# Kernel optimization log

Hardware: AMD Instinct MI355X
Metric: run time of the kernel (lower is better)

The kernel has to match this reference:

```python
import jax, jax.numpy as jnp
import numpy as np
from jax import lax

B, T, D = 2, 1024, 2048
HK, HV = 8, 16          # num key heads / num value heads
DK, DV = 128, 128       # head dims
KW = 4                  # conv kernel size
EPS = 1e-6
KEY_DIM = HK * DK
VALUE_DIM = HV * DV
CONV_DIM = 2 * KEY_DIM + VALUE_DIM


def setup_inputs() -> dict:
    key = jax.random.key(0)
    ks = jax.random.split(key, 9)
    w = lambda k, shape, s=0.02: jax.random.normal(k, shape, jnp.float32) * s
    return {
        'hidden_states': jax.random.normal(ks[0], (B, T, D), jnp.float32),
        'W_qkv': w(ks[1], (D, CONV_DIM)),
        'W_z': w(ks[2], (D, VALUE_DIM)),
        'W_b': w(ks[3], (D, HV)),
        'W_a': w(ks[4], (D, HV)),
        'conv_w': w(ks[5], (CONV_DIM, KW), 0.5),
        'dt_bias': jnp.ones((HV,), jnp.float32),
        'A_log': jnp.log(jax.random.uniform(ks[6], (HV,), jnp.float32, 1e-3, 16.0)),
        'norm_weight': jnp.ones((DV,), jnp.float32),
        'W_out': w(ks[7], (VALUE_DIM, D)),
    }


def _causal_conv_silu(x, w):
    # x: [B, C, T], w: [C, K] depthwise causal conv + SiLU (causal_conv1d_fn)
    k = w.shape[1]
    xp = jnp.pad(x, ((0, 0), (0, 0), (k - 1, 0)))
    y = sum(w[:, j][None, :, None] * xp[:, :, j:j + x.shape[2]] for j in range(k))
    return jax.nn.silu(y)


def _l2norm(x):
    return x * lax.rsqrt(jnp.sum(x * x, -1, keepdims=True) + 1e-6)


def reference(hidden_states, W_qkv, W_z, W_b, W_a, conv_w, dt_bias, A_log,
              norm_weight, W_out):
    Bb, Tt, _ = hidden_states.shape
    mixed = hidden_states @ W_qkv                       # [B,T,conv_dim]
    mixed = _causal_conv_silu(mixed.transpose(0, 2, 1), conv_w).transpose(0, 2, 1)
    q, k, v = jnp.split(mixed, [KEY_DIM, 2 * KEY_DIM], axis=-1)
    q = q.reshape(Bb, Tt, HK, DK)
    k = k.reshape(Bb, Tt, HK, DK)
    v = v.reshape(Bb, Tt, HV, DV)
    z = (hidden_states @ W_z).reshape(Bb, Tt, HV, DV)
    beta = jax.nn.sigmoid(hidden_states @ W_b)          # [B,T,HV]
    g = -jnp.exp(A_log) * jax.nn.softplus(hidden_states @ W_a + dt_bias)  # [B,T,HV]

    rep = HV // HK  # GQA: repeat_interleave q,k heads
    q = jnp.repeat(q, rep, axis=2)
    k = jnp.repeat(k, rep, axis=2)
    q = _l2norm(q) * (DK ** -0.5)                       # use_qk_l2norm + scale
    k = _l2norm(k)

    # gated delta-rule recurrence (fp32 state), scanned over time
    qs = q.transpose(1, 0, 2, 3)   # [T,B,HV,DK]
    ks = k.transpose(1, 0, 2, 3)
    vs = v.transpose(1, 0, 2, 3)   # [T,B,HV,DV]
    gs = g.transpose(1, 0, 2)      # [T,B,HV]
    bs = beta.transpose(1, 0, 2)

    def step(S, inp):
        qt, kt, vt, gt, bt = inp
        S = S * jnp.exp(gt)[..., None, None]                          # decay
        v_adj = (vt - jnp.einsum('bhk,bhkv->bhv', kt, S)) * bt[..., None]
        S = S + kt[..., None] * v_adj[..., None, :]                   # rank-1 delta update
        o = jnp.einsum('bhk,bhkv->bhv', qt, S)
        return S, o

    S0 = jnp.zeros((Bb, HV, DK, DV), jnp.float32)
    _, o = lax.scan(step, S0, (qs, ks, vs, gs, bs))
    o = o.transpose(1, 0, 2, 3)                         # [B,T,HV,DV]

    # gated RMSNorm over head_v_dim
    var = jnp.mean(o * o, -1, keepdims=True)
    o = o * lax.rsqrt(var + EPS) * norm_weight
    o = o * jax.nn.silu(z)

    return o.reshape(Bb, Tt, VALUE_DIM) @ W_out         # [B,T,D]
```

## Files before the change

kernel.cpp:

```cpp
#include <hip/hip_runtime.h>
#include <hip/hip_bf16.h>

#define B_ 2
#define T_ 1024
#define D_ 2048
#define HK_ 8
#define HV_ 16
#define DK_ 128
#define DV_ 128
#define KEY_DIM_ 1024
#define VALUE_DIM_ 2048
#define CONV_DIM_ 4096
#define BT_ 2048
#define NCH_ 16
#define CL_ 64

typedef __attribute__((ext_vector_type(8))) short short8;
typedef __attribute__((ext_vector_type(4))) float f32x4;

__device__ __forceinline__ short f2bf(float x) {
  __hip_bfloat16 h = __float2bfloat16(x);
  return *reinterpret_cast<short*>(&h);
}
__device__ __forceinline__ float bf2f(short u) {
  unsigned int x = ((unsigned int)(unsigned short)u) << 16;
  return __int_as_float(x);
}

#define GLOAD_LDS16(g, l)                                             \
  __builtin_amdgcn_global_load_lds(                                   \
      (const __attribute__((address_space(1))) void*)(g),             \
      (__attribute__((address_space(3))) void*)(l), 16, 0, 0)

__global__ void transpose_cast(const float* __restrict__ W, short* __restrict__ WT, int R, int C) {
  __shared__ float tile[32][33];
  int tx = threadIdx.x, ty = threadIdx.y;
  int x = blockIdx.x * 32 + tx;
#pragma unroll
  for (int j = 0; j < 4; ++j) {
    int r = blockIdx.y * 32 + ty + j * 8;
    tile[ty + j * 8][tx] = W[(long)r * C + x];
  }
  __syncthreads();
  int ro = blockIdx.y * 32 + tx;
#pragma unroll
  for (int j = 0; j < 4; ++j) {
    int co = blockIdx.x * 32 + ty + j * 8;
    WT[(long)co * R + ro] = f2bf(tile[tx][ty + j * 8]);
  }
}

__global__ void interleave_ba(const float* __restrict__ Wb, const float* __restrict__ Wa,
                              float* __restrict__ Wba32) {
  int i = blockIdx.x * 256 + threadIdx.x;
  int c = i & 31, k = i >> 5;
  Wba32[i] = (c < 16) ? Wb[k * 16 + c] : Wa[k * 16 + (c - 16)];
}

__global__ __launch_bounds__(512) void gemm256_split(const short* __restrict__ A,
                                                     const short* __restrict__ Bt,
                                                     float* __restrict__ C0,
                                                     float* __restrict__ C1,
                                                     int N0, int N1, int K) {
  __shared__ short lds[65536];
  const int tid = threadIdx.x;
  const int lane = tid & 63, wid = tid >> 6;
  const int quad = lane >> 4, l16 = lane & 15;
  const int wm = (wid >> 2) * 128, wn = (wid & 3) * 64;
  const int m0 = blockIdx.y * 256, n0 = blockIdx.x * 256;

  const int r8 = tid >> 3, t8 = (tid & 7) * 8;
  const int csw = t8 ^ ((r8 & 7) << 3);
  const int rB = (r8 & 31) + ((r8 >> 5) << 6);
  const int cswr = (quad ^ (l16 & 7)) << 3;
  const int NT = K >> 6, NIT = NT >> 1;

  f32x4 acc[8][4] = {};
  short8 a[4][2], bl[2][2], bh[2][2];

#define SGA(p, kt, rb)                                                        \
  GLOAD_LDS16(A + (long)(m0 + (rb) + r8) * K + (kt) * 64 + csw,               \
              lds + (p) * 32768 + ((rb) + r8) * 64 + t8)
#define SGB(p, kt, rb)                                                        \
  GLOAD_LDS16(Bt + (long)(n0 + (rb) + rB) * K + (kt) * 64 + csw,              \
              lds + (p) * 32768 + 16384 + ((rb) + rB) * 64 + t8)
#define UA0(p, kt) do { SGA(p, kt, 0);  SGA(p, kt, 128); } while (0)
#define UA2(p, kt) do { SGA(p, kt, 64); SGA(p, kt, 192); } while (0)
#define UB1(p, kt) do { SGB(p, kt, 0);  SGB(p, kt, 128); } while (0)
#define UB3(p, kt) do { SGB(p, kt, 32); SGB(p, kt, 160); } while (0)
#define RDA(p, r, kk) (*(const short8*)(lds + (p) * 32768 + (r) * 64 + (cswr ^ ((kk) << 5))))
#define RDB(p, r, kk) (*(const short8*)(lds + (p) * 32768 + 16384 + (r) * 64 + (cswr ^ ((kk) << 5))))
#define MFMA_(d, x, y) d = __builtin_amdgcn_mfma_f32_16x16x32_bf16(x, y, d, 0, 0, 0)
#define BAR_() do { __builtin_amdgcn_s_barrier(); __builtin_amdgcn_sched_barrier(0); } while (0)
#define PRIO_ON_() __builtin_amdgcn_s_setprio(1)
#define PRIO_OFF_() do { __builtin_amdgcn_s_setprio(0); __builtin_amdgcn_sched_barrier(0); } while (0)

  UA0(0, 0); UB1(0, 0); UA2(0, 0); UB3(0, 0);
  UA0(1, 1); UB1(1, 1); UA2(1, 1);
  asm volatile("s_waitcnt vmcnt(6)" ::: "memory");
  BAR_();

#pragma unroll 1
  for (int i = 0; i < NIT; ++i) {
    const int tb = 2 * i + 1, tc = 2 * i + 2, td = 2 * i + 3;
    const bool more = (i + 1 < NIT);

#pragma unroll
    for (int mi = 0; mi < 4; ++mi) {
      a[mi][0] = RDA(0, wm + mi * 16 + l16, 0);
      a[mi][1] = RDA(0, wm + mi * 16 + l16, 1);
    }
#pragma unroll
    for (int ni = 0; ni < 2; ++ni) {
      bl[ni][0] = RDB(0, wn + ni * 16 + l16, 0);
      bl[ni][1] = RDB(0, wn + ni * 16 + l16, 1);
    }
    UB3(1, tb);
    BAR_();
    PRIO_ON_();
#pragma unroll
    for (int mi = 0; mi < 4; ++mi)
#pragma unroll
      for (int ni = 0; ni < 2; ++ni) {
        MFMA_(acc[mi][ni], a[mi][0], bl[ni][0]);
        MFMA_(acc[mi][ni], a[mi][1], bl[ni][1]);
      }
    PRIO_OFF_();
    __builtin_amdgcn_s_barrier();

    __builtin_amdgcn_sched_barrier(0);
#pragma unroll
    for (int ni = 0; ni < 2; ++ni) {
      bh[ni][0] = RDB(0, wn + 32 + ni * 16 + l16, 0);
      bh[ni][1] = RDB(0, wn + 32 + ni * 16 + l16, 1);
    }
    if (more) UA0(0, tc);
    BAR_();
    PRIO_ON_();
#pragma unroll
    for (int mi = 0; mi < 4; ++mi)
#pragma unroll
      for (int ni = 0; ni < 2; ++ni) {
        MFMA_(acc[mi][2 + ni], a[mi][0], bh[ni][0]);
        MFMA_(acc[mi][2 + ni], a[mi][1], bh[ni][1]);
      }
    PRIO_OFF_();
    __builtin_amdgcn_s_barrier();

    __builtin_amdgcn_sched_barrier(0);
#pragma unroll
    for (int mi = 0; mi < 4; ++mi) {
      a[mi][0] = RDA(0, wm + 64 + mi * 16 + l16, 0);
      a[mi][1] = RDA(0, wm + 64 + mi * 16 + l16, 1);
    }
    if (more) UB1(0, tc);
    BAR_();
    PRIO_ON_();
#pragma unroll
    for (int mi = 0; mi < 4; ++mi)
#pragma unroll
      for (int ni = 0; ni < 2; ++ni) {
        MFMA_(acc[4 + mi][2 + ni], a[mi][0], bh[ni][0]);
        MFMA_(acc[4 + mi][2 + ni], a[mi][1], bh[ni][1]);
      }
    PRIO_OFF_();
    __builtin_amdgcn_s_barrier();

    __builtin_amdgcn_sched_barrier(0);
    if (more) UA2(0, tc);
    BAR_();
    PRIO_ON_();
#pragma unroll
    for (int mi = 0; mi < 4; ++mi)
#pragma unroll
      for (int ni = 0; ni < 2; ++ni) {
        MFMA_(acc[4 + mi][ni], a[mi][0], bl[ni][0]);
        MFMA_(acc[4 + mi][ni], a[mi][1], bl[ni][1]);
      }
    PRIO_OFF_();
    if (more) { asm volatile("s_waitcnt vmcnt(6)" ::: "memory"); }
    else      { asm volatile("s_waitcnt vmcnt(0)" ::: "memory"); }
    __builtin_amdgcn_s_barrier();

    __builtin_amdgcn_sched_barrier(0);
#pragma unroll
    for (int mi = 0; mi < 4; ++mi) {
      a[mi][0] = RDA(1, wm + mi * 16 + l16, 0);
      a[mi][1] = RDA(1, wm + mi * 16 + l16, 1);
    }
#pragma unroll
    for (int ni = 0; ni < 2; ++ni) {
      bl[ni][0] = RDB(1, wn + ni * 16 + l16, 0);
      bl[ni][1] = RDB(1, wn + ni * 16 + l16, 1);
    }
    if (more) UB3(0, tc);
    BAR_();
    PRIO_ON_();
#pragma unroll
    for (int mi = 0; mi < 4; ++mi)
#pragma unroll
      for (int ni = 0; ni < 2; ++ni) {
        MFMA_(acc[mi][ni], a[mi][0], bl[ni][0]);
        MFMA_(acc[mi][ni], a[mi][1], bl[ni][1]);
      }
    PRIO_OFF_();
    __builtin_amdgcn_s_barrier();

    __builtin_amdgcn_sched_barrier(0);
#pragma unroll
    for (int ni = 0; ni < 2; ++ni) {
      bh[ni][0] = RDB(1, wn + 32 + ni * 16 + l16, 0);
      bh[ni][1] = RDB(1, wn + 32 + ni * 16 + l16, 1);
    }
    if (more) UA0(1, td);
    BAR_();
    PRIO_ON_();
#pragma unroll
    for (int mi = 0; mi < 4; ++mi)
#pragma unroll
      for (int ni = 0; ni < 2; ++ni) {
        MFMA_(acc[mi][2 + ni], a[mi][0], bh[ni][0]);
        MFMA_(acc[mi][2 + ni], a[mi][1], bh[ni][1]);
      }
    PRIO_OFF_();
    __builtin_amdgcn_s_barrier();

    __builtin_amdgcn_sched_barrier(0);
#pragma unroll
    for (int mi = 0; mi < 4; ++mi) {
      a[mi][0] = RDA(1, wm + 64 + mi * 16 + l16, 0);
      a[mi][1] = RDA(1, wm + 64 + mi * 16 + l16, 1);
    }
    if (more) UB1(1, td);
    BAR_();
    PRIO_ON_();
#pragma unroll
    for (int mi = 0; mi < 4; ++mi)
#pragma unroll
      for (int ni = 0; ni < 2; ++ni) {
        MFMA_(acc[4 + mi][2 + ni], a[mi][0], bh[ni][0]);
        MFMA_(acc[4 + mi][2 + ni], a[mi][1], bh[ni][1]);
      }
    PRIO_OFF_();
    __builtin_amdgcn_s_barrier();

    __builtin_amdgcn_sched_barrier(0);
    if (more) UA2(1, td);
    BAR_();
    PRIO_ON_();
#pragma unroll
    for (int mi = 0; mi < 4; ++mi)
#pragma unroll
      for (int ni = 0; ni < 2; ++ni) {
        MFMA_(acc[4 + mi][ni], a[mi][0], bl[ni][0]);
        MFMA_(acc[4 + mi][ni], a[mi][1], bl[ni][1]);
      }
    PRIO_OFF_();
    if (more) { asm volatile("s_waitcnt vmcnt(6)" ::: "memory"); }
    else      { asm volatile("s_waitcnt vmcnt(0)" ::: "memory"); }
    __builtin_amdgcn_s_barrier();
    __builtin_amdgcn_sched_barrier(0);
  }

  float* Cw; int ldc, cb;
  if (n0 < N0) { Cw = C0; ldc = N0; cb = n0; }
  else         { Cw = C1; ldc = N1; cb = n0 - N0; }
#pragma unroll
  for (int mi = 0; mi < 8; ++mi)
#pragma unroll
    for (int ni = 0; ni < 4; ++ni)
#pragma unroll
      for (int r = 0; r < 4; ++r) {
        int row = m0 + wm + mi * 16 + quad * 4 + r;
        int col = cb + wn + ni * 16 + l16;
        Cw[(long)row * ldc + col] = acc[mi][ni][r];
      }
#undef SGA
#undef SGB
#undef UA0
#undef UA2
#undef UB1
#undef UB3
#undef RDA
#undef RDB
#undef MFMA_
#undef BAR_
#undef PRIO_ON_
#undef PRIO_OFF_
}

__global__ __launch_bounds__(256) void gemm128_ks(const short* __restrict__ A,
                                                  const short* __restrict__ Bt,
                                                  float* __restrict__ Cp,
                                                  int M, int N, int K) {
  __shared__ short As[2][128 * 32];
  __shared__ short Bs[2][128 * 32];
  int m0 = blockIdx.y * 128, n0 = blockIdx.x * 128;
  int kh = K >> 1;
  int kbeg = blockIdx.z * kh;
  int tid = threadIdx.x;
  int wave = tid >> 6, lane = tid & 63;
  int wm = (wave >> 1) * 64, wn = (wave & 1) * 64;
  int quad = lane >> 4, l16 = lane & 15;
  f32x4 acc[4][4] = {};

  int ar = tid >> 2;
  int ac = (tid & 3) * 8;
  const short* Ag0 = A + (long)(m0 + ar) * K + ac + kbeg;
  const short* Ag1 = A + (long)(m0 + 64 + ar) * K + ac + kbeg;
  const short* Bg0 = Bt + (long)(n0 + ar) * K + ac + kbeg;
  const short* Bg1 = Bt + (long)(n0 + 64 + ar) * K + ac + kbeg;
  int NT = kh >> 5;

#define STAGE_(t, c)                                  \
  do {                                                \
    GLOAD_LDS16(Ag0 + (t) * 32, As[c] + tid * 8);     \
    GLOAD_LDS16(Ag1 + (t) * 32, As[c] + 64 * 32 + tid * 8); \
    GLOAD_LDS16(Bg0 + (t) * 32, Bs[c] + tid * 8);     \
    GLOAD_LDS16(Bg1 + (t) * 32, Bs[c] + 64 * 32 + tid * 8); \
  } while (0)

  STAGE_(0, 0);
  STAGE_(1, 1);

  for (int t = 0; t < NT; ++t) {
    int c = t & 1;
    if (t + 1 < NT) {
      asm volatile("s_waitcnt vmcnt(4)" ::: "memory");
    } else {
      asm volatile("s_waitcnt vmcnt(0)" ::: "memory");
    }
    __builtin_amdgcn_s_barrier();
    __builtin_amdgcn_sched_barrier(0);

    short8 af[4], bf_[4];
#pragma unroll
    for (int i = 0; i < 4; ++i) af[i] = *(const short8*)(As[c] + (wm + i * 16 + l16) * 32 + quad * 8);
#pragma unroll
    for (int j = 0; j < 4; ++j) bf_[j] = *(const short8*)(Bs[c] + (wn + j * 16 + l16) * 32 + quad * 8);
#pragma unroll
    for (int i = 0; i < 4; ++i)
#pragma unroll
      for (int j = 0; j < 4; ++j)
        acc[i][j] = __builtin_amdgcn_mfma_f32_16x16x32_bf16(af[i], bf_[j], acc[i][j], 0, 0, 0);

    __builtin_amdgcn_sched_barrier(0);
    __builtin_amdgcn_s_barrier();
    if (t + 2 < NT) STAGE_(t + 2, c);
  }

  float* Cz = Cp + (long)blockIdx.z * M * N;
#pragma unroll
  for (int i = 0; i < 4; ++i)
#pragma unroll
    for (int j = 0; j < 4; ++j)
#pragma unroll
      for (int r = 0; r < 4; ++r) {
        int row = m0 + wm + i * 16 + quad * 4 + r;
        int colx = n0 + wn + j * 16 + l16;
        Cz[(long)row * N + colx] = acc[i][j][r];
      }
#undef STAGE_
}

__global__ void add2(const float* __restrict__ p0, const float* __restrict__ p1,
                     float* __restrict__ out, int n4) {
  int i = blockIdx.x * 256 + threadIdx.x;
  if (i < n4) {
    float4 a = ((const float4*)p0)[i];
    float4 b = ((const float4*)p1)[i];
    float4 o;
    o.x = a.x + b.x; o.y = a.y + b.y; o.z = a.z + b.z; o.w = a.w + b.w;
    ((float4*)out)[i] = o;
  }
}

__global__ __launch_bounds__(256) void small_proj(const float* __restrict__ hidden,
                                                  const float* __restrict__ Wba32,
                                                  const float* __restrict__ dt_bias,
                                                  const float* __restrict__ A_log,
                                                  float* __restrict__ betaT,
                                                  float* __restrict__ gT,
                                                  short* __restrict__ hbf) {
  __shared__ float red[2][32][33];
  int r0 = blockIdx.x * 2;
  int tid = threadIdx.x;
  int cg = tid & 7, s = tid >> 3;
  const f32x4* wp = (const f32x4*)Wba32 + (long)s * 64 * 8 + cg;
  const f32x4* h0 = (const f32x4*)(hidden + (long)r0 * D_ + s * 64);
  const f32x4* h1 = (const f32x4*)(hidden + (long)(r0 + 1) * D_ + s * 64);
  f32x4 a0 = {0.f, 0.f, 0.f, 0.f}, a1 = {0.f, 0.f, 0.f, 0.f};
#pragma unroll
  for (int ii = 0; ii < 16; ++ii) {
    f32x4 ha = h0[ii], hb = h1[ii];
    f32x4 w0 = wp[(ii * 4 + 0) * 8];
    f32x4 w1 = wp[(ii * 4 + 1) * 8];
    f32x4 w2 = wp[(ii * 4 + 2) * 8];
    f32x4 w3 = wp[(ii * 4 + 3) * 8];
    a0 += ha[0] * w0; a1 += hb[0] * w0;
    a0 += ha[1] * w1; a1 += hb[1] * w1;
    a0 += ha[2] * w2; a1 += hb[2] * w2;
    a0 += ha[3] * w3; a1 += hb[3] * w3;
  }
#pragma unroll
  for (int j = 0; j < 4; ++j) {
    red[0][s][cg * 4 + j] = a0[j];
    red[1][s][cg * 4 + j] = a1[j];
  }
  {
    int colb = s * 64 + cg * 8;
    const float* p0 = hidden + (long)r0 * D_ + colb;
    const float* p1 = p0 + D_;
    float4 x0 = *(const float4*)(p0);
    float4 x1 = *(const float4*)(p0 + 4);
    float4 y0 = *(const float4*)(p1);
    float4 y1 = *(const float4*)(p1 + 4);
    short8 o0, o1;
    o0[0] = f2bf(x0.x); o0[1] = f2bf(x0.y); o0[2] = f2bf(x0.z); o0[3] = f2bf(x0.w);
    o0[4] = f2bf(x1.x); o0[5] = f2bf(x1.y); o0[6] = f2bf(x1.z); o0[7] = f2bf(x1.w);
    o1[0] = f2bf(y0.x); o1[1] = f2bf(y0.y); o1[2] = f2bf(y0.z); o1[3] = f2bf(y0.w);
    o1[4] = f2bf(y1.x); o1[5] = f2bf(y1.y); o1[6] = f2bf(y1.z); o1[7] = f2bf(y1.w);
    *(short8*)(hbf + (long)r0 * D_ + colb) = o0;
    *(short8*)(hbf + (long)(r0 + 1) * D_ + colb) = o1;
  }
  __syncthreads();
  if (tid < 64) {
    int row = tid >> 5, c = tid & 31;
    float t0 = 0.f, t1 = 0.f, t2 = 0.f, t3 = 0.f;
#pragma unroll
    for (int ss = 0; ss < 32; ss += 4) {
      t0 += red[row][ss][c];
      t1 += red[row][ss + 1][c];
      t2 += red[row][ss + 2][c];
      t3 += red[row][ss + 3][c];
    }
    float t = (t0 + t1) + (t2 + t3);
    int r = r0 + row;
    if (c < 16) {
      betaT[c * BT_ + r] = 1.f / (1.f + __expf(-t));
    } else {
      int hh = c - 16;
      float y = t + dt_bias[hh];
      float sp = fmaxf(y, 0.f) + log1pf(__expf(-fabsf(y)));
      gT[hh * BT_ + r] = -__expf(A_log[hh]) * sp;
    }
  }
}

__global__ void conv_silu(const float* __restrict__ x, const float* __restrict__ w,
                          float* __restrict__ y) {
  int idx = blockIdx.x * 256 + threadIdx.x;
  int c = idx & (CONV_DIM_ - 1);
  int bt = idx >> 12;
  int t = bt & (T_ - 1);
  float4 wc = *(const float4*)(w + c * 4);
  const float* xp = x + (long)idx;
  float acc = wc.w * xp[0];
  if (t >= 1) acc += wc.z * xp[-CONV_DIM_];
  if (t >= 2) acc += wc.y * xp[-2 * CONV_DIM_];
  if (t >= 3) acc += wc.x * xp[-3 * CONV_DIM_];
  y[idx] = acc * (1.f / (1.f + __expf(-acc)));
}

__global__ __launch_bounds__(64) void qknorm(const float* __restrict__ qkv,
                                             short* __restrict__ qb, short* __restrict__ kb) {
  int bi = blockIdx.x;
  int which = bi & 1;
  int h = (bi >> 1) & 7;
  int bt = bi >> 4;
  int lane = threadIdx.x;
  const float* src = qkv + (long)bt * CONV_DIM_ + which * KEY_DIM_ + h * DK_;
  float2 v = *(const float2*)(src + lane * 2);
  float ss = v.x * v.x + v.y * v.y;
#pragma unroll
  for (int m = 32; m; m >>= 1) ss += __shfl_xor(ss, m, 64);
  float scale = rsqrtf(ss + 1e-6f);
  if (which == 0) scale *= 0.08838834764831845f;
  short* dst = (which ? kb : qb) + ((long)bt * HK_ + h) * DK_;
  short2 o; o.x = f2bf(v.x * scale); o.y = f2bf(v.y * scale);
  ((short2*)dst)[lane] = o;
}

__global__ __launch_bounds__(256, 2) void chunk_phase1(
    const short* __restrict__ qbf, const short* __restrict__ kbf,
    const float* __restrict__ qkv, const float* __restrict__ gT,
    const float* __restrict__ bT,
    short* __restrict__ Pm, short* __restrict__ GQ, short* __restrict__ KtT,
    short* __restrict__ Wneg, float* __restrict__ Ut, float* __restrict__ Gammac) {
  __shared__ float Al[64 * 64];
  __shared__ float Gs[64], Gam[64], Dd[64], Bet[64], BG[64];

  int ci = blockIdx.x;
  int c = ci & 15, hv = (ci >> 4) & 15, b = ci >> 8;
  int hk = hv >> 1;
  int t0 = c * CL_;
  int tid = threadIdx.x;
  int wave = tid >> 6, lane = tid & 63, quad = lane >> 4, l16 = lane & 15;

  if (tid < 64) {
    float g = gT[(hv * B_ + b) * T_ + t0 + tid];
    float x = g;
#pragma unroll
    for (int off = 1; off < 64; off <<= 1) {
      float y = __shfl_up(x, off, 64);
      if (tid >= off) x += y;
    }
    Gs[tid] = x;
    float gm = __expf(x);
    Gam[tid] = gm;
    float Gtot = __shfl(x, 63, 64);
    Dd[tid] = __expf(Gtot - x);
    float bb = bT[(hv * B_ + b) * T_ + t0 + tid];
    Bet[tid] = bb;
    BG[tid] = bb * gm;
    if (tid == 63) Gammac[ci] = __expf(x);
// ... 151 lines not shown
      for (int kk = 0; kk < 4; ++kk)
        Wn[kk] = *(const short8*)(Wneg + cj * 8192 + (16 * wave + l16) * 128 + kk * 32 + quad * 8);
      const float* up = Ut + cj * 8192 + (16 * wave + quad * 4) * 128 + n0 + l16;
#pragma unroll
      for (int r = 0; r < 4; ++r) Un[r] = up[r * 128];
#pragma unroll
      for (int kk = 0; kk < 2; ++kk)
#pragma unroll
        for (int i = 0; i < 2; ++i)
          Kn[kk][i] = *(const short8*)(KtT + cj * 8192 + (32 * wave + 16 * i + l16) * 64 + kk * 32 + quad * 8);
    }
    __syncthreads();
    f32x4 Ua = Ur;
#pragma unroll
    for (int kk = 0; kk < 4; ++kk) {
      short8 bfv = *(const short8*)(SLT + l16 * 136 + kk * 32 + quad * 8);
      Ua = __builtin_amdgcn_mfma_f32_16x16x32_bf16(Wr[kk], bfv, Ua, 0, 0, 0);
    }
    {
      int s0 = 16 * wave + quad * 4;
      short4 p;
      p.x = f2bf(Ua[0]); p.y = f2bf(Ua[1]); p.z = f2bf(Ua[2]); p.w = f2bf(Ua[3]);
      *(short4*)(ULT + l16 * 72 + s0) = p;
      *(short4*)(UTg + ci * 8192 + (n0 + l16) * 64 + s0) = p;
    }
    __syncthreads();
    float gc = Gammac[ci];
#pragma unroll
    for (int i = 0; i < 2; ++i)
#pragma unroll
      for (int r = 0; r < 4; ++r) S2[i][r] *= gc;
#pragma unroll
    for (int kk = 0; kk < 2; ++kk) {
      short8 bfv = *(const short8*)(ULT + l16 * 72 + kk * 32 + quad * 8);
#pragma unroll
      for (int i = 0; i < 2; ++i)
        S2[i] = __builtin_amdgcn_mfma_f32_16x16x32_bf16(Kr[kk][i], bfv, S2[i], 0, 0, 0);
    }
    __syncthreads();
    if (ch + 1 < NCH_) {
#pragma unroll
      for (int kk = 0; kk < 4; ++kk) Wr[kk] = Wn[kk];
      Ur = Un;
#pragma unroll
      for (int kk = 0; kk < 2; ++kk)
#pragma unroll
        for (int i = 0; i < 2; ++i) Kr[kk][i] = Kn[kk][i];
    }
  }
}

__global__ __launch_bounds__(256) void chunk_phase3(
    const short* __restrict__ GQ, const short* __restrict__ ScTg,
    const short* __restrict__ Pm, const short* __restrict__ UTg,
    const float* __restrict__ zbuf, const float* __restrict__ nw,
    short* __restrict__ obf) {
  int ci = blockIdx.x;
  int c = ci & 15, hv = (ci >> 4) & 15, b = ci >> 8;
  int t0 = c * CL_;
  int tid = threadIdx.x, wave = tid >> 6, lane = tid & 63, quad = lane >> 4, l16 = lane & 15;
  f32x4 acc[8] = {};
#pragma unroll
  for (int kk = 0; kk < 4; ++kk) {
    short8 af = *(const short8*)(GQ + (long)ci * 8192 + (16 * wave + l16) * 128 + kk * 32 + quad * 8);
#pragma unroll
    for (int j = 0; j < 8; ++j) {
      short8 bfv = *(const short8*)(ScTg + (long)ci * 16384 + (16 * j + l16) * 128 + kk * 32 + quad * 8);
      acc[j] = __builtin_amdgcn_mfma_f32_16x16x32_bf16(af, bfv, acc[j], 0, 0, 0);
    }
  }
#pragma unroll
  for (int kk = 0; kk < 2; ++kk) {
    short8 af = *(const short8*)(Pm + (long)ci * 4096 + (16 * wave + l16) * 64 + kk * 32 + quad * 8);
#pragma unroll
    for (int j = 0; j < 8; ++j) {
      short8 bfv = *(const short8*)(UTg + (long)ci * 8192 + (16 * j + l16) * 64 + kk * 32 + quad * 8);
      acc[j] = __builtin_amdgcn_mfma_f32_16x16x32_bf16(af, bfv, acc[j], 0, 0, 0);
    }
  }
#pragma unroll
  for (int r = 0; r < 4; ++r) {
    float ss = 0.f;
#pragma unroll
    for (int j = 0; j < 8; ++j) ss += acc[j][r] * acc[j][r];
    ss += __shfl_xor(ss, 1, 64);
    ss += __shfl_xor(ss, 2, 64);
    ss += __shfl_xor(ss, 4, 64);
    ss += __shfl_xor(ss, 8, 64);
    float scale = rsqrtf(ss * (1.f / 128.f) + 1e-6f);
    int t = t0 + 16 * wave + quad * 4 + r;
    long base = (long)(b * T_ + t) * VALUE_DIM_ + hv * DV_;
#pragma unroll
    for (int j = 0; j < 8; ++j) {
      int n = 16 * j + l16;
      float zv = zbuf[base + n];
      float sz = zv * (1.f / (1.f + __expf(-zv)));
      obf[base + n] = f2bf(acc[j][r] * scale * nw[n] * sz);
    }
  }
}

extern "C" void kernel_launch(void* const* d_in, const int* in_sizes, int n_in,
                              void* d_out, int out_size, void* d_ws, size_t ws_size,
                              hipStream_t stream) {
  const float* hidden  = (const float*)d_in[0];
  const float* W_qkv   = (const float*)d_in[1];
  const float* W_z     = (const float*)d_in[2];
  const float* W_b     = (const float*)d_in[3];
  const float* W_a     = (const float*)d_in[4];
  const float* conv_w  = (const float*)d_in[5];
  const float* dt_bias = (const float*)d_in[6];
  const float* A_log   = (const float*)d_in[7];
  const float* norm_w  = (const float*)d_in[8];
  const float* W_out   = (const float*)d_in[9];
  float* out = (float*)d_out;

  char* ws = (char*)d_ws;
  size_t off = 0;
  auto alloc = [&](size_t bytes) {
    void* p = ws + off;
    off += (bytes + 255) & ~(size_t)255;
    return p;
  };
  short* hidden_bf = (short*)alloc((size_t)BT_ * D_ * 2);
  short* WcatT     = (short*)alloc((size_t)(CONV_DIM_ + VALUE_DIM_) * D_ * 2);
  short* WoutT     = (short*)alloc((size_t)D_ * VALUE_DIM_ * 2);
  float* mixed     = (float*)alloc((size_t)BT_ * CONV_DIM_ * 4);
  float* qkv       = (float*)alloc((size_t)BT_ * CONV_DIM_ * 4);
  float* zbuf      = (float*)alloc((size_t)BT_ * VALUE_DIM_ * 4);
  short* qbf       = (short*)alloc((size_t)BT_ * KEY_DIM_ * 2);
  short* kbf       = (short*)alloc((size_t)BT_ * KEY_DIM_ * 2);
  float* betab     = (float*)alloc((size_t)BT_ * HV_ * 4);
  float* gb        = (float*)alloc((size_t)BT_ * HV_ * 4);
  float* Wba32     = (float*)alloc((size_t)D_ * 32 * 4);
  short* Wneg      = (short*)alloc((size_t)512 * 8192 * 2);
  float* Ut32      = (float*)alloc((size_t)512 * 8192 * 4);
  short* KtT       = (short*)alloc((size_t)512 * 8192 * 2);
  short* UTg       = (short*)alloc((size_t)512 * 8192 * 2);
  short* ScTg      = (short*)alloc((size_t)512 * 16384 * 2);
  float* Gammac    = (float*)alloc((size_t)512 * 4);
  short* Pm   = (short*)(mixed + (size_t)BT_ * VALUE_DIM_);
  short* GQ   = Pm + (size_t)512 * 4096;
  short* obf  = hidden_bf;
  float* Cpart = qkv;

  dim3 tb32(32, 8);
  transpose_cast<<<dim3(CONV_DIM_ / 32, D_ / 32), tb32, 0, stream>>>(W_qkv, WcatT, D_, CONV_DIM_);
  transpose_cast<<<dim3(VALUE_DIM_ / 32, D_ / 32), tb32, 0, stream>>>(W_z, WcatT + (size_t)CONV_DIM_ * D_, D_, VALUE_DIM_);
  transpose_cast<<<dim3(D_ / 32, VALUE_DIM_ / 32), tb32, 0, stream>>>(W_out, WoutT, VALUE_DIM_, D_);
  interleave_ba<<<32 * D_ / 256, 256, 0, stream>>>(W_b, W_a, Wba32);

  small_proj<<<BT_ / 2, 256, 0, stream>>>(hidden, Wba32, dt_bias, A_log, betab, gb, hidden_bf);

  gemm256_split<<<dim3((CONV_DIM_ + VALUE_DIM_) / 256, BT_ / 256), 512, 0, stream>>>(
      hidden_bf, WcatT, mixed, zbuf, CONV_DIM_, VALUE_DIM_, D_);
  conv_silu<<<BT_ * CONV_DIM_ / 256, 256, 0, stream>>>(mixed, conv_w, qkv);
  qknorm<<<BT_ * HK_ * 2, 64, 0, stream>>>(qkv, qbf, kbf);

  chunk_phase1<<<512, 256, 0, stream>>>(qbf, kbf, qkv, gb, betab, Pm, GQ, KtT, Wneg, Ut32, Gammac);
  chunk_phase2<<<256, 256, 0, stream>>>(Wneg, Ut32, KtT, Gammac, UTg, ScTg);
  chunk_phase3<<<512, 256, 0, stream>>>(GQ, ScTg, Pm, UTg, zbuf, norm_w, obf);

  gemm128_ks<<<dim3(D_ / 128, BT_ / 128, 2), 256, 0, stream>>>(obf, WoutT, Cpart, BT_, D_, VALUE_DIM_);
  add2<<<(BT_ * D_ / 4 + 255) / 256, 256, 0, stream>>>(Cpart, Cpart + (size_t)BT_ * D_, out, BT_ * D_ / 4);
}
```

Baseline: 379.2 us.

## Retile input GEMM to 256x192 and port output GEMM to pipelined 256x128 kernel

The fused QKV/Z projection GEMM now uses 256x192 tiles instead of 256x256. That gives 32x8=256 blocks rather than 24x8=192, for better CU coverage on the device, with a per-column split when writing to the two outputs. The output projection replaces the simple 128x128 double-buffered split-K kernel with a 512-thread 256x128 version of the swizzled, barrier-phased pipeline. The cost is a smaller per-block reuse ratio, a more complex staging schedule, and tuned vmcnt counts that must match the number of loads in flight.

```diff
diff --git a/kernel.cpp b/kernel.cpp
--- a/kernel.cpp
+++ b/kernel.cpp
@@ -57,46 +57,42 @@
   Wba32[i] = (c < 16) ? Wb[k * 16 + c] : Wa[k * 16 + (c - 16)];
 }
 
-__global__ __launch_bounds__(512) void gemm256_split(const short* __restrict__ A,
-                                                     const short* __restrict__ Bt,
-                                                     float* __restrict__ C0,
-                                                     float* __restrict__ C1,
-                                                     int N0, int N1, int K) {
-  __shared__ short lds[65536];
-  const int tid = threadIdx.x;
-  const int lane = tid & 63, wid = tid >> 6;
-  const int quad = lane >> 4, l16 = lane & 15;
-  const int wm = (wid >> 2) * 128, wn = (wid & 3) * 64;
-  const int m0 = blockIdx.y * 256, n0 = blockIdx.x * 256;
-
-  const int r8 = tid >> 3, t8 = (tid & 7) * 8;
-  const int csw = t8 ^ ((r8 & 7) << 3);
-  const int rB = (r8 & 31) + ((r8 >> 5) << 6);
-  const int cswr = (quad ^ (l16 & 7)) << 3;
-  const int NT = K >> 6, NIT = NT >> 1;
-
-  f32x4 acc[8][4] = {};
-  short8 a[4][2], bl[2][2], bh[2][2];
-
-#define SGA(p, kt, rb)                                                        \
-  GLOAD_LDS16(A + (long)(m0 + (rb) + r8) * K + (kt) * 64 + csw,               \
-              lds + (p) * 32768 + ((rb) + r8) * 64 + t8)
-#define SGB(p, kt, rb)                                                        \
-  GLOAD_LDS16(Bt + (long)(n0 + (rb) + rB) * K + (kt) * 64 + csw,              \
-              lds + (p) * 32768 + 16384 + ((rb) + rB) * 64 + t8)
-#define UA0(p, kt) do { SGA(p, kt, 0);  SGA(p, kt, 128); } while (0)
-#define UA2(p, kt) do { SGA(p, kt, 64); SGA(p, kt, 192); } while (0)
-#define UB1(p, kt) do { SGB(p, kt, 0);  SGB(p, kt, 128); } while (0)
-#define UB3(p, kt) do { SGB(p, kt, 32); SGB(p, kt, 160); } while (0)
-#define RDA(p, r, kk) (*(const short8*)(lds + (p) * 32768 + (r) * 64 + (cswr ^ ((kk) << 5))))
-#define RDB(p, r, kk) (*(const short8*)(lds + (p) * 32768 + 16384 + (r) * 64 + (cswr ^ ((kk) << 5))))
 #define MFMA_(d, x, y) d = __builtin_amdgcn_mfma_f32_16x16x32_bf16(x, y, d, 0, 0, 0)
 #define BAR_() do { __builtin_amdgcn_s_barrier(); __builtin_amdgcn_sched_barrier(0); } while (0)
 #define PRIO_ON_() __builtin_amdgcn_s_setprio(1)
 #define PRIO_OFF_() do { __builtin_amdgcn_s_setprio(0); __builtin_amdgcn_sched_barrier(0); } while (0)
 
-  UA0(0, 0); UB1(0, 0); UA2(0, 0); UB3(0, 0);
-  UA0(1, 1); UB1(1, 1); UA2(1, 1);
+__global__ __launch_bounds__(512) void gemm256n192(const short* __restrict__ A,
+                                                   const short* __restrict__ Bt,
+                                                   float* __restrict__ C0,
+                                                   float* __restrict__ C1,
+                                                   int N0, int N1, int K) {
+  __shared__ short lds[57344];
+  const int tid = threadIdx.x;
+  const int lane = tid & 63, wid = tid >> 6;
+  const int quad = lane >> 4, l16 = lane & 15;
+  const int wm = (wid >> 1) * 64, wn = (wid & 1) * 96;
+  const int m0 = blockIdx.y * 256, n0 = blockIdx.x * 192;
+
+  const int r8 = tid >> 3, t8 = (tid & 7) * 8;
+  const int csw = t8 ^ ((r8 & 7) << 3);
+  const int cswr = (quad ^ (l16 & 7)) << 3;
+  const int NIT = K >> 7;
+
+  f32x4 acc[4][6] = {};
+  short8 a[4][2], bl[3][2], bh[3][2];
+
+#define SGA(p, kt, rb) GLOAD_LDS16(A + (long)(m0 + (rb) + r8) * K + (kt) * 64 + csw, \
+                                   lds + (p) * 28672 + ((rb) + r8) * 64 + t8)
+#define SGB(p, kt, rb) GLOAD_LDS16(Bt + (long)(n0 + (rb) + r8) * K + (kt) * 64 + csw, \
+                                   lds + (p) * 28672 + 16384 + ((rb) + r8) * 64 + t8)
+#define RDA(p, r, kk) (*(const short8*)(lds + (p) * 28672 + (r) * 64 + (cswr ^ ((kk) << 5))))
+#define RDB(p, r, kk) (*(const short8*)(lds + (p) * 28672 + 16384 + (r) * 64 + (cswr ^ ((kk) << 5))))
+
+  SGA(0, 0, 0); SGA(0, 0, 64); SGA(0, 0, 128); SGA(0, 0, 192);
+  SGB(0, 0, 0); SGB(0, 0, 64); SGB(0, 0, 128);
+  SGA(1, 1, 0); SGA(1, 1, 64); SGA(1, 1, 128); SGA(1, 1, 192);
+  SGB(1, 1, 0); SGB(1, 1, 64);
   asm volatile("s_waitcnt vmcnt(6)" ::: "memory");
   BAR_();
 
@@ -106,7 +102,220 @@
     const bool more = (i + 1 < NIT);
 
 #pragma unroll
-    for (int mi = 0; mi < 4; ++mi) {
+    for (int mi = 0; mi < 2; ++mi) {
+      a[mi][0] = RDA(0, wm + mi * 16 + l16, 0);
+      a[mi][1] = RDA(0, wm + mi * 16 + l16, 1);
+    }
+#pragma unroll
+    for (int ni = 0; ni < 3; ++ni) {
+      bl[ni][0] = RDB(0, wn + ni * 16 + l16, 0);
+      bl[ni][1] = RDB(0, wn + ni * 16 + l16, 1);
+    }
+    SGB(1, tb, 128);
+    BAR_();
+    PRIO_ON_();
+#pragma unroll
+    for (int mi = 0; mi < 2; ++mi)
+#pragma unroll
+      for (int ni = 0; ni < 3; ++ni) {
+        MFMA_(acc[mi][ni], a[mi][0], bl[ni][0]);
+        MFMA_(acc[mi][ni], a[mi][1], bl[ni][1]);
+      }
+    PRIO_OFF_();
+    __builtin_amdgcn_s_barrier();
+
+    __builtin_amdgcn_sched_barrier(0);
+#pragma unroll
+    for (int mi = 2; mi < 4; ++mi) {
+      a[mi][0] = RDA(0, wm + mi * 16 + l16, 0);
+      a[mi][1] = RDA(0, wm + mi * 16 + l16, 1);
+    }
+    BAR_();
+    PRIO_ON_();
+#pragma unroll
+    for (int mi = 2; mi < 4; ++mi)
+#pragma unroll
+      for (int ni = 0; ni < 3; ++ni) {
+        MFMA_(acc[mi][ni], a[mi][0], bl[ni][0]);
+        MFMA_(acc[mi][ni], a[mi][1], bl[ni][1]);
+      }
+    PRIO_OFF_();
+    __builtin_amdgcn_s_barrier();
+
+    __builtin_amdgcn_sched_barrier(0);
+#pragma unroll
+    for (int ni = 0; ni < 3; ++ni) {
+      bh[ni][0] = RDB(0, wn + 48 + ni * 16 + l16, 0);
+      bh[ni][1] = RDB(0, wn + 48 + ni * 16 + l16, 1);
+    }
+    if (more) { SGA(0, tc, 0); SGA(0, tc, 64); }
+    BAR_();
+    PRIO_ON_();
+#pragma unroll
+    for (int mi = 0; mi < 2; ++mi)
+#pragma unroll
+      for (int ni = 0; ni < 3; ++ni) {
+        MFMA_(acc[mi][3 + ni], a[mi][0], bh[ni][0]);
+        MFMA_(acc[mi][3 + ni], a[mi][1], bh[ni][1]);
+      }
+    PRIO_OFF_();
+    __builtin_amdgcn_s_barrier();
+
+    __builtin_amdgcn_sched_barrier(0);
+    if (more) { SGA(0, tc, 128); SGA(0, tc, 192); SGB(0, tc, 0); SGB(0, tc, 64); }
+    BAR_();
+    PRIO_ON_();
+#pragma unroll
+    for (int mi = 2; mi < 4; ++mi)
+#pragma unroll
+      for (int ni = 0; ni < 3; ++ni) {
+        MFMA_(acc[mi][3 + ni], a[mi][0], bh[ni][0]);
+        MFMA_(acc[mi][3 + ni], a[mi][1], bh[ni][1]);
+      }
+    PRIO_OFF_();
+    if (more) { asm volatile("s_waitcnt vmcnt(6)" ::: "memory"); }
+    else      { asm volatile("s_waitcnt vmcnt(0)" ::: "memory"); }
+    __builtin_amdgcn_s_barrier();
+
+    __builtin_amdgcn_sched_barrier(0);
+#pragma unroll
+    for (int mi = 0; mi < 2; ++mi) {
+      a[mi][0] = RDA(1, wm + mi * 16 + l16, 0);
+      a[mi][1] = RDA(1, wm + mi * 16 + l16, 1);
+    }
+#pragma unroll
+    for (int ni = 0; ni < 3; ++ni) {
+      bl[ni][0] = RDB(1, wn + ni * 16 + l16, 0);
+      bl[ni][1] = RDB(1, wn + ni * 16 + l16, 1);
+    }
+    if (more) SGB(0, tc, 128);
+    BAR_();
+    PRIO_ON_();
+#pragma unroll
+    for (int mi = 0; mi < 2; ++mi)
+#pragma unroll
+      for (int ni = 0; ni < 3; ++ni) {
+        MFMA_(acc[mi][ni], a[mi][0], bl[ni][0]);
+        MFMA_(acc[mi][ni], a[mi][1], bl[ni][1]);
+      }
+    PRIO_OFF_();
+    __builtin_amdgcn_s_barrier();
+
+    __builtin_amdgcn_sched_barrier(0);
+#pragma unroll
+    for (int mi = 2; mi < 4; ++mi) {
+      a[mi][0] = RDA(1, wm + mi * 16 + l16, 0);
+      a[mi][1] = RDA(1, wm + mi * 16 + l16, 1);
+    }
+    BAR_();
+    PRIO_ON_();
+#pragma unroll
+    for (int mi = 2; mi < 4; ++mi)
+#pragma unroll
+      for (int ni = 0; ni < 3; ++ni) {
+        MFMA_(acc[mi][ni], a[mi][0], bl[ni][0]);
+        MFMA_(acc[mi][ni], a[mi][1], bl[ni][1]);
+      }
+    PRIO_OFF_();
+    __builtin_amdgcn_s_barrier();
+
+    __builtin_amdgcn_sched_barrier(0);
+#pragma unroll
+    for (int ni = 0; ni < 3; ++ni) {
+      bh[ni][0] = RDB(1, wn + 48 + ni * 16 + l16, 0);
+      bh[ni][1] = RDB(1, wn + 48 + ni * 16 + l16, 1);
+    }
+    if (more) { SGA(1, td, 0); SGA(1, td, 64); }
+    BAR_();
+    PRIO_ON_();
+#pragma unroll
+    for (int mi = 0; mi < 2; ++mi)
+#pragma unroll
+      for (int ni = 0; ni < 3; ++ni) {
+        MFMA_(acc[mi][3 + ni], a[mi][0], bh[ni][0]);
+        MFMA_(acc[mi][3 + ni], a[mi][1], bh[ni][1]);
+      }
+    PRIO_OFF_();
+    __builtin_amdgcn_s_barrier();
+
+    __builtin_amdgcn_sched_barrier(0);
+    if (more) { SGA(1, td, 128); SGA(1, td, 192); SGB(1, td, 0); SGB(1, td, 64); }
+    BAR_();
+    PRIO_ON_();
+#pragma unroll
+    for (int mi = 2; mi < 4; ++mi)
+#pragma unroll
+      for (int ni = 0; ni < 3; ++ni) {
+        MFMA_(acc[mi][3 + ni], a[mi][0], bh[ni][0]);
+        MFMA_(acc[mi][3 + ni], a[mi][1], bh[ni][1]);
+      }
+    PRIO_OFF_();
+    if (more) { asm volatile("s_waitcnt vmcnt(6)" ::: "memory"); }
+    else      { asm volatile("s_waitcnt vmcnt(0)" ::: "memory"); }
+    __builtin_amdgcn_s_barrier();
+    __builtin_amdgcn_sched_barrier(0);
+  }
+
+#pragma unroll
+  for (int mi = 0; mi < 4; ++mi)
+#pragma unroll
+    for (int ni = 0; ni < 6; ++ni)
+#pragma unroll
+      for (int r = 0; r < 4; ++r) {
+        int row = m0 + wm + mi * 16 + quad * 4 + r;
+        int col = n0 + wn + ni * 16 + l16;
+        if (col < N0) C0[(long)row * N0 + col] = acc[mi][ni][r];
+        else          C1[(long)row * N1 + (col - N0)] = acc[mi][ni][r];
+      }
+#undef SGA
+#undef SGB
+#undef RDA
+#undef RDB
+}
+
+__global__ __launch_bounds__(512) void gemm256ks(const short* __restrict__ Ag,
+                                                 const short* __restrict__ Btg,
+                                                 float* __restrict__ Cp,
+                                                 int M, int N, int K) {
+  __shared__ short lds[49152];
+  const int tid = threadIdx.x;
+  const int lane = tid & 63, wid = tid >> 6;
+  const int quad = lane >> 4, l16 = lane & 15;
+  const int wm = (wid >> 1) * 64, wn = (wid & 1) * 64;
+  const int m0 = blockIdx.y * 256, n0 = blockIdx.x * 128;
+  const int kh = K >> 1;
+  const short* A = Ag + blockIdx.z * kh;
+  const short* Bt = Btg + blockIdx.z * kh;
+
+  const int r8 = tid >> 3, t8 = (tid & 7) * 8;
+  const int csw = t8 ^ ((r8 & 7) << 3);
+  const int cswr = (quad ^ (l16 & 7)) << 3;
+  const int NIT = kh >> 7;
+
+  f32x4 acc[4][4] = {};
+  short8 a[4][2], bl[2][2], bh[2][2];
+
+#define SGA(p, kt, rb) GLOAD_LDS16(A + (long)(m0 + (rb) + r8) * K + (kt) * 64 + csw, \
+                                   lds + (p) * 24576 + ((rb) + r8) * 64 + t8)
+#define SGB(p, kt, rb) GLOAD_LDS16(Bt + (long)(n0 + (rb) + r8) * K + (kt) * 64 + csw, \
+                                   lds + (p) * 24576 + 16384 + ((rb) + r8) * 64 + t8)
+#define RDA(p, r, kk) (*(const short8*)(lds + (p) * 24576 + (r) * 64 + (cswr ^ ((kk) << 5))))
+#define RDB(p, r, kk) (*(const short8*)(lds + (p) * 24576 + 16384 + (r) * 64 + (cswr ^ ((kk) << 5))))
+
+  SGA(0, 0, 0); SGA(0, 0, 64); SGA(0, 0, 128); SGA(0, 0, 192);
+  SGB(0, 0, 0); SGB(0, 0, 64);
+  SGA(1, 1, 0); SGA(1, 1, 64); SGA(1, 1, 128); SGA(1, 1, 192);
+  SGB(1, 1, 0);
+  asm volatile("s_waitcnt vmcnt(5)" ::: "memory");
+  BAR_();
+
+#pragma unroll 1
+  for (int i = 0; i < NIT; ++i) {
+    const int tb = 2 * i + 1, tc = 2 * i + 2, td = 2 * i + 3;
+    const bool more = (i + 1 < NIT);
+
+#pragma unroll
+    for (int mi = 0; mi < 2; ++mi) {
       a[mi][0] = RDA(0, wm + mi * 16 + l16, 0);
       a[mi][1] = RDA(0, wm + mi * 16 + l16, 1);
     }
@@ -115,11 +324,11 @@
       bl[ni][0] = RDB(0, wn + ni * 16 + l16, 0);
       bl[ni][1] = RDB(0, wn + ni * 16 + l16, 1);
     }
-    UB3(1, tb);
-    BAR_();
-    PRIO_ON_();
-#pragma unroll
-    for (int mi = 0; mi < 4; ++mi)
+    SGB(1, tb, 64);
+    BAR_();
+    PRIO_ON_();
+#pragma unroll
+    for (int mi = 0; mi < 2; ++mi)
 #pragma unroll
       for (int ni = 0; ni < 2; ++ni) {
         MFMA_(acc[mi][ni], a[mi][0], bl[ni][0]);
@@ -130,15 +339,33 @@
 
     __builtin_amdgcn_sched_barrier(0);
 #pragma unroll
+    for (int mi = 2; mi < 4; ++mi) {
+      a[mi][0] = RDA(0, wm + mi * 16 + l16, 0);
+      a[mi][1] = RDA(0, wm + mi * 16 + l16, 1);
+    }
+    BAR_();
+    PRIO_ON_();
+#pragma unroll
+    for (int mi = 2; mi < 4; ++mi)
+#pragma unroll
+      for (int ni = 0; ni < 2; ++ni) {
+        MFMA_(acc[mi][ni], a[mi][0], bl[ni][0]);
+        MFMA_(acc[mi][ni], a[mi][1], bl[ni][1]);
+      }
+    PRIO_OFF_();
+    __builtin_amdgcn_s_barrier();
+
+    __builtin_amdgcn_sched_barrier(0);
+#pragma unroll
     for (int ni = 0; ni < 2; ++ni) {
       bh[ni][0] = RDB(0, wn + 32 + ni * 16 + l16, 0);
       bh[ni][1] = RDB(0, wn + 32 + ni * 16 + l16, 1);
     }
-    if (more) UA0(0, tc);
-    BAR_();
-    PRIO_ON_();
-#pragma unroll
-    for (int mi = 0; mi < 4; ++mi)
+    if (more) { SGA(0, tc, 0); SGA(0, tc, 64); }
+    BAR_();
+    PRIO_ON_();
+#pragma unroll
+    for (int mi = 0; mi < 2; ++mi)
 #pragma unroll
       for (int ni = 0; ni < 2; ++ni) {
         MFMA_(acc[mi][2 + ni], a[mi][0], bh[ni][0]);
@@ -148,43 +375,24 @@
     __builtin_amdgcn_s_barrier();
 
     __builtin_amdgcn_sched_barrier(0);
-#pragma unroll
-    for (int mi = 0; mi < 4; ++mi) {
-      a[mi][0] = RDA(0, wm + 64 + mi * 16 + l16, 0);
-      a[mi][1] = RDA(0, wm + 64 + mi * 16 + l16, 1);
-    }
-    if (more) UB1(0, tc);
-    BAR_();
-    PRIO_ON_();
-#pragma unroll
-    for (int mi = 0; mi < 4; ++mi)
+    if (more) { SGA(0, tc, 128); SGA(0, tc, 192); SGB(0, tc, 0); }
+    BAR_();
+    PRIO_ON_();
+#pragma unroll
+    for (int mi = 2; mi < 4; ++mi)
 #pragma unroll
       for (int ni = 0; ni < 2; ++ni) {
-        MFMA_(acc[4 + mi][2 + ni], a[mi][0], bh[ni][0]);
-        MFMA_(acc[4 + mi][2 + ni], a[mi][1], bh[ni][1]);
-      }
-    PRIO_OFF_();
-    __builtin_amdgcn_s_barrier();
-
-    __builtin_amdgcn_sched_barrier(0);
-    if (more) UA2(0, tc);
-    BAR_();
-    PRIO_ON_();
-#pragma unroll
-    for (int mi = 0; mi < 4; ++mi)
-#pragma unroll
-      for (int ni = 0; ni < 2; ++ni) {
-        MFMA_(acc[4 + mi][ni], a[mi][0], bl[ni][0]);
-        MFMA_(acc[4 + mi][ni], a[mi][1], bl[ni][1]);
-      }
-    PRIO_OFF_();
-    if (more) { asm volatile("s_waitcnt vmcnt(6)" ::: "memory"); }
+        MFMA_(acc[mi][2 + ni], a[mi][0], bh[ni][0]);
+        MFMA_(acc[mi][2 + ni], a[mi][1], bh[ni][1]);
+      }
+    PRIO_OFF_();
+    if (more) { asm volatile("s_waitcnt vmcnt(5)" ::: "memory"); }
     else      { asm volatile("s_waitcnt vmcnt(0)" ::: "memory"); }
     __builtin_amdgcn_s_barrier();
 
     __builtin_amdgcn_sched_barrier(0);
 #pragma unroll
-    for (int mi = 0; mi < 4; ++mi) {
+    for (int mi = 0; mi < 2; ++mi) {
       a[mi][0] = RDA(1, wm + mi * 16 + l16, 0);
       a[mi][1] = RDA(1, wm + mi * 16 + l16, 1);
     }
@@ -193,11 +401,11 @@
       bl[ni][0] = RDB(1, wn + ni * 16 + l16, 0);
       bl[ni][1] = RDB(1, wn + ni * 16 + l16, 1);
     }
-    if (more) UB3(0, tc);
-    BAR_();
-    PRIO_ON_();
-#pragma unroll
-    for (int mi = 0; mi < 4; ++mi)
+    if (more) SGB(0, tc, 64);
+    BAR_();
+    PRIO_ON_();
+#pragma unroll
+    for (int mi = 0; mi < 2; ++mi)
 #pragma unroll
       for (int ni = 0; ni < 2; ++ni) {
         MFMA_(acc[mi][ni], a[mi][0], bl[ni][0]);
@@ -208,15 +416,33 @@
 
     __builtin_amdgcn_sched_barrier(0);
 #pragma unroll
+    for (int mi = 2; mi < 4; ++mi) {
+      a[mi][0] = RDA(1, wm + mi * 16 + l16, 0);
+      a[mi][1] = RDA(1, wm + mi * 16 + l16, 1);
+    }
+    BAR_();
+    PRIO_ON_();
+#pragma unroll
+    for (int mi = 2; mi < 4; ++mi)
+#pragma unroll
+      for (int ni = 0; ni < 2; ++ni) {
+        MFMA_(acc[mi][ni], a[mi][0], bl[ni][0]);
+        MFMA_(acc[mi][ni], a[mi][1], bl[ni][1]);
+      }
+    PRIO_OFF_();
+    __builtin_amdgcn_s_barrier();
+
+    __builtin_amdgcn_sched_barrier(0);
+#pragma unroll
     for (int ni = 0; ni < 2; ++ni) {
       bh[ni][0] = RDB(1, wn + 32 + ni * 16 + l16, 0);
       bh[ni][1] = RDB(1, wn + 32 + ni * 16 + l16, 1);
     }
-    if (more) UA0(1, td);
-    BAR_();
-    PRIO_ON_();
-#pragma unroll
-    for (int mi = 0; mi < 4; ++mi)
+    if (more) { SGA(1, td, 0); SGA(1, td, 64); }
+    BAR_();
+    PRIO_ON_();
+#pragma unroll
+    for (int mi = 0; mi < 2; ++mi)
 #pragma unroll
       for (int ni = 0; ni < 2; ++ni) {
         MFMA_(acc[mi][2 + ni], a[mi][0], bh[ni][0]);
@@ -226,141 +452,38 @@
     __builtin_amdgcn_s_barrier();
 
     __builtin_amdgcn_sched_barrier(0);
-#pragma unroll
-    for (int mi = 0; mi < 4; ++mi) {
-      a[mi][0] = RDA(1, wm + 64 + mi * 16 + l16, 0);
-      a[mi][1] = RDA(1, wm + 64 + mi * 16 + l16, 1);
-    }
-    if (more) UB1(1, td);
-    BAR_();
-    PRIO_ON_();
-#pragma unroll
-    for (int mi = 0; mi < 4; ++mi)
+    if (more) { SGA(1, td, 128); SGA(1, td, 192); SGB(1, td, 0); }
+    BAR_();
+    PRIO_ON_();
+#pragma unroll
+    for (int mi = 2; mi < 4; ++mi)
 #pragma unroll
       for (int ni = 0; ni < 2; ++ni) {
-        MFMA_(acc[4 + mi][2 + ni], a[mi][0], bh[ni][0]);
-        MFMA_(acc[4 + mi][2 + ni], a[mi][1], bh[ni][1]);
-      }
-    PRIO_OFF_();
-    __builtin_amdgcn_s_barrier();
-
-    __builtin_amdgcn_sched_barrier(0);
-    if (more) UA2(1, td);
-    BAR_();
-    PRIO_ON_();
-#pragma unroll
-    for (int mi = 0; mi < 4; ++mi)
-#pragma unroll
-      for (int ni = 0; ni < 2; ++ni) {
-        MFMA_(acc[4 + mi][ni], a[mi][0], bl[ni][0]);
-        MFMA_(acc[4 + mi][ni], a[mi][1], bl[ni][1]);
-      }
-    PRIO_OFF_();
-    if (more) { asm volatile("s_waitcnt vmcnt(6)" ::: "memory"); }
+        MFMA_(acc[mi][2 + ni], a[mi][0], bh[ni][0]);
+        MFMA_(acc[mi][2 + ni], a[mi][1], bh[ni][1]);
+      }
+    PRIO_OFF_();
+    if (more) { asm volatile("s_waitcnt vmcnt(5)" ::: "memory"); }
     else      { asm volatile("s_waitcnt vmcnt(0)" ::: "memory"); }
     __builtin_amdgcn_s_barrier();
     __builtin_amdgcn_sched_barrier(0);
   }
 
-  float* Cw; int ldc, cb;
-  if (n0 < N0) { Cw = C0; ldc = N0; cb = n0; }
-  else         { Cw = C1; ldc = N1; cb = n0 - N0; }
-#pragma unroll
-  for (int mi = 0; mi < 8; ++mi)
+  float* Cz = Cp + (long)blockIdx.z * M * N;
+#pragma unroll
+  for (int mi = 0; mi < 4; ++mi)
 #pragma unroll
     for (int ni = 0; ni < 4; ++ni)
 #pragma unroll
       for (int r = 0; r < 4; ++r) {
         int row = m0 + wm + mi * 16 + quad * 4 + r;
-        int col = cb + wn + ni * 16 + l16;
-        Cw[(long)row * ldc + col] = acc[mi][ni][r];
+        int col = n0 + wn + ni * 16 + l16;
+        Cz[(long)row * N + col] = acc[mi][ni][r];
       }
 #undef SGA
 #undef SGB
-#undef UA0
-#undef UA2
-#undef UB1
-#undef UB3
 #undef RDA
 #undef RDB
-#undef MFMA_
-#undef BAR_
-#undef PRIO_ON_
-#undef PRIO_OFF_
-}
-
-__global__ __launch_bounds__(256) void gemm128_ks(const short* __restrict__ A,
-                                                  const short* __restrict__ Bt,
-                                                  float* __restrict__ Cp,
-                                                  int M, int N, int K) {
-  __shared__ short As[2][128 * 32];
-  __shared__ short Bs[2][128 * 32];
-  int m0 = blockIdx.y * 128, n0 = blockIdx.x * 128;
-  int kh = K >> 1;
-  int kbeg = blockIdx.z * kh;
-  int tid = threadIdx.x;
-  int wave = tid >> 6, lane = tid & 63;
-  int wm = (wave >> 1) * 64, wn = (wave & 1) * 64;
-  int quad = lane >> 4, l16 = lane & 15;
-  f32x4 acc[4][4] = {};
-
-  int ar = tid >> 2;
-  int ac = (tid & 3) * 8;
-  const short* Ag0 = A + (long)(m0 + ar) * K + ac + kbeg;
-  const short* Ag1 = A + (long)(m0 + 64 + ar) * K + ac + kbeg;
-  const short* Bg0 = Bt + (long)(n0 + ar) * K + ac + kbeg;
-  const short* Bg1 = Bt + (long)(n0 + 64 + ar) * K + ac + kbeg;
-  int NT = kh >> 5;
-
-#define STAGE_(t, c)                                  \
-  do {                                                \
-    GLOAD_LDS16(Ag0 + (t) * 32, As[c] + tid * 8);     \
-    GLOAD_LDS16(Ag1 + (t) * 32, As[c] + 64 * 32 + tid * 8); \
-    GLOAD_LDS16(Bg0 + (t) * 32, Bs[c] + tid * 8);     \
-    GLOAD_LDS16(Bg1 + (t) * 32, Bs[c] + 64 * 32 + tid * 8); \
-  } while (0)
-
-  STAGE_(0, 0);
-  STAGE_(1, 1);
-
-  for (int t = 0; t < NT; ++t) {
-    int c = t & 1;
-    if (t + 1 < NT) {
-      asm volatile("s_waitcnt vmcnt(4)" ::: "memory");
-    } else {
-      asm volatile("s_waitcnt vmcnt(0)" ::: "memory");
-    }
-    __builtin_amdgcn_s_barrier();
-    __builtin_amdgcn_sched_barrier(0);
-
-    short8 af[4], bf_[4];
-#pragma unroll
-    for (int i = 0; i < 4; ++i) af[i] = *(const short8*)(As[c] + (wm + i * 16 + l16) * 32 + quad * 8);
-#pragma unroll
-    for (int j = 0; j < 4; ++j) bf_[j] = *(const short8*)(Bs[c] + (wn + j * 16 + l16) * 32 + quad * 8);
-#pragma unroll
-    for (int i = 0; i < 4; ++i)
-#pragma unroll
-      for (int j = 0; j < 4; ++j)
-        acc[i][j] = __builtin_amdgcn_mfma_f32_16x16x32_bf16(af[i], bf_[j], acc[i][j], 0, 0, 0);
-
-    __builtin_amdgcn_sched_barrier(0);
-    __builtin_amdgcn_s_barrier();
-    if (t + 2 < NT) STAGE_(t + 2, c);
-  }
-
-  float* Cz = Cp + (long)blockIdx.z * M * N;
-#pragma unroll
-  for (int i = 0; i < 4; ++i)
-#pragma unroll
-    for (int j = 0; j < 4; ++j)
-#pragma unroll
-      for (int r = 0; r < 4; ++r) {
-        int row = m0 + wm + i * 16 + quad * 4 + r;
-        int colx = n0 + wn + j * 16 + l16;
-        Cz[(long)row * N + colx] = acc[i][j][r];
-      }
-#undef STAGE_
 }
 
 __global__ void add2(const float* __restrict__ p0, const float* __restrict__ p1,
@@ -818,7 +941,7 @@
 
   small_proj<<<BT_ / 2, 256, 0, stream>>>(hidden, Wba32, dt_bias, A_log, betab, gb, hidden_bf);
 
-  gemm256_split<<<dim3((CONV_DIM_ + VALUE_DIM_) / 256, BT_ / 256), 512, 0, stream>>>(
+  gemm256n192<<<dim3((CONV_DIM_ + VALUE_DIM_) / 192, BT_ / 256), 512, 0, stream>>>(
       hidden_bf, WcatT, mixed, zbuf, CONV_DIM_, VALUE_DIM_, D_);
   conv_silu<<<BT_ * CONV_DIM_ / 256, 256, 0, stream>>>(mixed, conv_w, qkv);
   qknorm<<<BT_ * HK_ * 2, 64, 0, stream>>>(qkv, qbf, kbf);
@@ -827,6 +950,6 @@
   chunk_phase2<<<256, 256, 0, stream>>>(Wneg, Ut32, KtT, Gammac, UTg, ScTg);
   chunk_phase3<<<512, 256, 0, stream>>>(GQ, ScTg, Pm, UTg, zbuf, norm_w, obf);
 
-  gemm128_ks<<<dim3(D_ / 128, BT_ / 128, 2), 256, 0, stream>>>(obf, WoutT, Cpart, BT_, D_, VALUE_DIM_);
+  gemm256ks<<<dim3(D_ / 128, BT_ / 256, 2), 512, 0, stream>>>(obf, WoutT, Cpart, BT_, D_, VALUE_DIM_);
   add2<<<(BT_ * D_ / 4 + 255) / 256, 256, 0, stream>>>(Cpart, Cpart + (size_t)BT_ * D_, out, BT_ * D_ / 4);
 }
```

After: 364.9 us. 3.8% less time.
